# Optimization experiments

Measured on AMD Instinct MI355X. Metric: run time of the kernel, lower is better.

## Reference

```python
import jax, jax.numpy as jnp
import numpy as np

T, B, E, H = 1024, 64, 512, 512


def setup_inputs() -> dict:
    key = jax.random.key(0)
    ks = jax.random.split(key, 13)
    a = 1.0 / np.sqrt(H)
    u = lambda k, shape, lo=-a, hi=a: jax.random.uniform(k, shape, jnp.float32, lo, hi)
    return {
        "embeds": jax.random.normal(ks[0], (T, B, E), jnp.float32),
        "w_gx": u(ks[1], (E, H)), "w_gh": u(ks[2], (H, H)), "bias_g": u(ks[3], (H,)),
        "w_ix": u(ks[4], (E, H)), "w_ih": u(ks[5], (H, H)), "bias_i": u(ks[6], (H,)),
        "w_fx": u(ks[7], (E, H)), "w_fh": u(ks[8], (H, H)), "bias_f": u(ks[9], (H,), 1.0 - a, 1.0 + a),
        "w_ox": u(ks[10], (E, H)), "w_oh": u(ks[11], (H, H)), "bias_o": u(ks[12], (H,)),
    }


def reference(embeds, w_gx, w_gh, bias_g, w_ix, w_ih, bias_i,
              w_fx, w_fh, bias_f, w_ox, w_oh, bias_o):
    # Precompute all input projections in one big batched matmul: [T,B,4H]
    Wx = jnp.concatenate([w_gx, w_ix, w_fx, w_ox], axis=1)            # [E,4H]
    Wh = jnp.concatenate([w_gh, w_ih, w_fh, w_oh], axis=1)            # [H,4H]
    b = jnp.concatenate([bias_g, bias_i, bias_f, bias_o], axis=0)     # [4H]
    x_proj = jnp.einsum("tbe,ef->tbf", embeds, Wx) + b                # [T,B,4H]

    Bsz = embeds.shape[1]
    h0 = jnp.zeros((Bsz, H), embeds.dtype)
    c0 = jnp.zeros((Bsz, H), embeds.dtype)

    def step(carry, xp):
        h, c = carry
        z = xp + h @ Wh                                               # [B,4H]
        g = jnp.tanh(z[:, :H])
        i = jax.nn.sigmoid(z[:, H:2 * H])
        f = jax.nn.sigmoid(z[:, 2 * H:3 * H])
        o = jax.nn.sigmoid(z[:, 3 * H:])
        c_new = g * i + c * f
        h_new = jnp.tanh(c_new) * o
        return (h_new, c_new), h_new

    _, hs = jax.lax.scan(step, (h0, c0), x_proj)
    return hs  # [T,B,H]
```

## Files before the change

### kernel.cpp

```cpp
#include <hip/hip_runtime.h>
#include <stdint.h>
#include <stddef.h>


#define Tn 1024
#define Bn 64
#define Hn 512
#define En 512
#define NGROUP 4
#define NJBLK 32
#define NBLOCK (NGROUP * NJBLK)
#define POISON8 0x7F807F807F807F80ull
#define INIT8   0xAAAAAAAAAAAAAAAAull

using bf16x8 = __attribute__((ext_vector_type(8))) __bf16;
using f32x4  = __attribute__((ext_vector_type(4))) float;
using u16x8  = __attribute__((ext_vector_type(8))) unsigned short;
using u16x4  = __attribute__((ext_vector_type(4))) unsigned short;

__device__ __forceinline__ unsigned short f2bf(float f) {
    unsigned u = __builtin_bit_cast(unsigned, f);
    unsigned r = (u + 0x7FFFu + ((u >> 16) & 1u)) >> 16;
    return (unsigned short)r;
}
__device__ __forceinline__ float bf2f(unsigned short b) {
    unsigned u = ((unsigned)b) << 16;
    return __builtin_bit_cast(float, u);
}

__global__ __launch_bounds__(256, 1) void lstm_persistent(
    const float* __restrict__ embeds,
    const float* __restrict__ wx0, const float* __restrict__ wh0, const float* __restrict__ bs0,
    const float* __restrict__ wx1, const float* __restrict__ wh1, const float* __restrict__ bs1,
    const float* __restrict__ wx2, const float* __restrict__ wh2, const float* __restrict__ bs2,
    const float* __restrict__ wx3, const float* __restrict__ wh3, const float* __restrict__ bs3,
    float* __restrict__ out, void* __restrict__ ws)
{
    __shared__ unsigned short Xhi[16][520];
    __shared__ unsigned short Xlo[16][520];
    __shared__ unsigned short Hl[16][520];
    __shared__ float exch[4][16][17];

    const int tid  = threadIdx.x;
    const int wav  = tid >> 6;
    const int lane = tid & 63;
    const int q    = lane >> 4;
    const int n    = lane & 15;

    const int bidx = blockIdx.x;
    const int gid  = (bidx >> 1) & 3;
    const int kid  = ((bidx >> 3) << 1) | (bidx & 1);
    const int b0   = gid * 16;
    const int j0   = kid * 16;

    unsigned long long* gbase = (unsigned long long*)ws + (size_t)gid * 3 * 2048;

    const float* wxp = (wav == 0) ? wx0 : (wav == 1) ? wx1 : (wav == 2) ? wx2 : wx3;
    const float* whp = (wav == 0) ? wh0 : (wav == 1) ? wh1 : (wav == 2) ? wh2 : wh3;
    const float* bsp = (wav == 0) ? bs0 : (wav == 1) ? bs1 : (wav == 2) ? bs2 : bs3;

    bf16x8 WXhi[16], WXlo[16], WHhi[16], WHlo[16];
    const int col = j0 + n;
    #pragma unroll
    for (int kk = 0; kk < 16; ++kk) {
        u16x8 xh, xl, hh, hl;
        #pragma unroll
        for (int i = 0; i < 8; ++i) {
            int k = kk * 32 + q * 8 + i;
            float w  = wxp[(size_t)k * Hn + col];
            unsigned short hi = f2bf(w);
            xh[i] = hi;
            xl[i] = f2bf(w - bf2f(hi));
            w  = whp[(size_t)k * Hn + col];
            hi = f2bf(w);
            hh[i] = hi;
            hl[i] = f2bf(w - bf2f(hi));
        }
        WXhi[kk] = __builtin_bit_cast(bf16x8, xh);
        WXlo[kk] = __builtin_bit_cast(bf16x8, xl);
        WHhi[kk] = __builtin_bit_cast(bf16x8, hh);
        WHlo[kk] = __builtin_bit_cast(bf16x8, hl);
    }
    const float bias_l = bsp[col];
    float c_state = 0.f;
    const int b = tid >> 4, j = tid & 15;

    float4 xpre[8];
    #pragma unroll
    for (int it = 0; it < 8; ++it) {
        int idx = tid + it * 256;
        int r = idx >> 7, cc = idx & 127;
        xpre[it] = ((const float4*)(embeds + ((size_t)(b0 + r)) * En))[cc];
    }

    for (int t = 1; t <= Tn; ++t) {
        const int tau = t - 1;

        #pragma unroll
        for (int it = 0; it < 8; ++it) {
            int idx = tid + it * 256;
            int r = idx >> 7, cc = idx & 127;
            float4 v = xpre[it];
            float fs[4] = {v.x, v.y, v.z, v.w};
            u16x4 vh, vl;
            #pragma unroll
            for (int e = 0; e < 4; ++e) {
                unsigned short hb = f2bf(fs[e]);
                vh[e] = hb;
                vl[e] = f2bf(fs[e] - bf2f(hb));
            }
            *(u16x4*)&Xhi[r][cc * 4] = vh;
            *(u16x4*)&Xlo[r][cc * 4] = vl;
        }
        __syncthreads();

        unsigned long long hv8[8];
        unsigned long long* src = gbase + (size_t)((t - 1) % 3) * 2048;
        if (t > 1) {
            #pragma unroll
            for (int i = 0; i < 8; ++i)
                hv8[i] = __hip_atomic_load(src + tid + i * 256,
                                           __ATOMIC_RELAXED, __HIP_MEMORY_SCOPE_AGENT);
        }

        if (t < Tn) {
            #pragma unroll
            for (int it = 0; it < 8; ++it) {
                int idx = tid + it * 256;
                int r = idx >> 7, cc = idx & 127;
                xpre[it] = ((const float4*)(embeds + ((size_t)t * Bn + b0 + r) * En))[cc];
            }
        }

        f32x4 acc, acc2, acc3;
        acc[0] = bias_l; acc[1] = bias_l; acc[2] = bias_l; acc[3] = bias_l;
        acc2[0] = 0.f; acc2[1] = 0.f; acc2[2] = 0.f; acc2[3] = 0.f;
        acc3[0] = 0.f; acc3[1] = 0.f; acc3[2] = 0.f; acc3[3] = 0.f;

        #pragma unroll
        for (int kk = 0; kk < 16; ++kk) {
            bf16x8 ah = __builtin_bit_cast(bf16x8, *(const u16x8*)&Xhi[n][kk * 32 + q * 8]);
            bf16x8 al = __builtin_bit_cast(bf16x8, *(const u16x8*)&Xlo[n][kk * 32 + q * 8]);
            acc  = __builtin_amdgcn_mfma_f32_16x16x32_bf16(ah, WXhi[kk], acc, 0, 0, 0);
            acc2 = __builtin_amdgcn_mfma_f32_16x16x32_bf16(ah, WXlo[kk], acc2, 0, 0, 0);
            acc3 = __builtin_amdgcn_mfma_f32_16x16x32_bf16(al, WXhi[kk], acc3, 0, 0, 0);
        }

        if (t > 1) {
            int bad = 0;
            #pragma unroll
            for (int i = 0; i < 8; ++i)
                bad |= (hv8[i] == POISON8 || hv8[i] == INIT8) ? (1 << i) : 0;
            while (bad) {
                #pragma unroll
                for (int i = 0; i < 8; ++i)
                    if (bad & (1 << i))
                        hv8[i] = __hip_atomic_load(src + tid + i * 256,
                                                   __ATOMIC_RELAXED, __HIP_MEMORY_SCOPE_AGENT);
                int nb = 0;
                #pragma unroll
                for (int i = 0; i < 8; ++i)
                    nb |= (hv8[i] == POISON8 || hv8[i] == INIT8) ? (1 << i) : 0;
                bad = nb;
            }
            #pragma unroll
            for (int i = 0; i < 8; ++i) {
                int idx = tid + i * 256, r = idx >> 7, c8 = idx & 127;
                *(u16x4*)&Hl[r][c8 * 4] = __builtin_bit_cast(u16x4, hv8[i]);
            }
        }

        if (tid < 64) {
            int pr = tid >> 2, pq = tid & 3;
            __hip_atomic_store(gbase + (size_t)((t + 1) % 3) * 2048
                                   + pr * 128 + (j0 >> 2) + pq,
                               (unsigned long long)POISON8,
                               __ATOMIC_RELAXED, __HIP_MEMORY_SCOPE_AGENT);
        }

        if (t > 1) {
            __syncthreads();
            #pragma unroll
            for (int kk = 0; kk < 16; ++kk) {
                bf16x8 a = __builtin_bit_cast(bf16x8, *(const u16x8*)&Hl[n][kk * 32 + q * 8]);
                acc  = __builtin_amdgcn_mfma_f32_16x16x32_bf16(a, WHhi[kk], acc, 0, 0, 0);
                acc2 = __builtin_amdgcn_mfma_f32_16x16x32_bf16(a, WHlo[kk], acc2, 0, 0, 0);
            }
        }

        #pragma unroll
        for (int r = 0; r < 4; ++r) {
            float zv  = acc[r] + acc2[r] + acc3[r];
            float arg = (wav == 0) ? -2.f * zv : -zv;
            float s   = __builtin_amdgcn_rcpf(1.f + __expf(arg));
            float act = (wav == 0) ? (2.f * s - 1.f) : s;
            exch[wav][q * 4 + r][n] = act;
        }
        __syncthreads();

        float hv;
        {
            float g  = exch[0][b][j];
            float ig = exch[1][b][j];
            float fg = exch[2][b][j];
            float og = exch[3][b][j];
            c_state = g * ig + c_state * fg;
            float e2 = __expf(-2.f * c_state);
            float th = 2.f * __builtin_amdgcn_rcpf(1.f + e2) - 1.f;
            hv = th * og;
        }

        {
            unsigned pk = (unsigned)f2bf(hv);
            unsigned v1 = __shfl_down((int)pk, 1);
            unsigned v2 = __shfl_down((int)pk, 2);
            unsigned v3 = __shfl_down((int)pk, 3);
            if ((lane & 3) == 0 && t < Tn) {
                unsigned long long qv =
                    (unsigned long long)(pk | (v1 << 16))
                    | ((unsigned long long)(v2 | (v3 << 16)) << 32);
                __hip_atomic_store(gbase + (size_t)(t % 3) * 2048
                                       + b * 128 + (j0 >> 2) + (j >> 2),
                                   qv, __ATOMIC_RELAXED, __HIP_MEMORY_SCOPE_AGENT);
            }
        }

        out[((size_t)tau * Bn + b0 + b) * Hn + j0 + j] = hv;
    }
}

extern "C" void kernel_launch(void* const* d_in, const int* in_sizes, int n_in,
                              void* d_out, int out_size, void* d_ws, size_t ws_size,
                              hipStream_t stream) {
    lstm_persistent<<<dim3(NBLOCK), dim3(256), 0, stream>>>(
        (const float*)d_in[0],
        (const float*)d_in[1], (const float*)d_in[2], (const float*)d_in[3],
        (const float*)d_in[4], (const float*)d_in[5], (const float*)d_in[6],
        (const float*)d_in[7], (const float*)d_in[8], (const float*)d_in[9],
        (const float*)d_in[10], (const float*)d_in[11], (const float*)d_in[12],
        (float*)d_out, d_ws);
}
```

Baseline: 3.230 ms.

## Load hidden state straight into MFMA fragments and double-buffer the input tile

The global hidden-state exchange buffer is re-laid out in MFMA fragment order, so each lane atomically loads its own A-operand chunks into registers instead of staging them through shared memory. This drops the LDS write, a __syncthreads and the LDS reads from the recurrent path. The input embedding conversion is double-buffered one step ahead, which removes the per-step barrier before the X matmul. The hidden matmul also uses separate accumulators to shorten the dependency chain. In exchange, per-lane register pressure rises (32 u64 values) and the poll loop covers more loads.

```diff
diff --git a/kernel.cpp b/kernel.cpp
--- a/kernel.cpp
+++ b/kernel.cpp
@@ -17,6 +17,7 @@
 using f32x4  = __attribute__((ext_vector_type(4))) float;
 using u16x8  = __attribute__((ext_vector_type(8))) unsigned short;
 using u16x4  = __attribute__((ext_vector_type(4))) unsigned short;
+using u64x2  = __attribute__((ext_vector_type(2))) unsigned long long;
 
 __device__ __forceinline__ unsigned short f2bf(float f) {
     unsigned u = __builtin_bit_cast(unsigned, f);
@@ -26,6 +27,9 @@
 __device__ __forceinline__ float bf2f(unsigned short b) {
     unsigned u = ((unsigned)b) << 16;
     return __builtin_bit_cast(float, u);
+}
+__device__ __forceinline__ int chunk_idx(int c, int b) {
+    return ((c >> 5) << 7) + (((c >> 3) & 3) << 5) + (b << 1) + ((c >> 2) & 1);
 }
 
 __global__ __launch_bounds__(256, 1) void lstm_persistent(
@@ -36,9 +40,8 @@
     const float* __restrict__ wx3, const float* __restrict__ wh3, const float* __restrict__ bs3,
     float* __restrict__ out, void* __restrict__ ws)
 {
-    __shared__ unsigned short Xhi[16][520];
-    __shared__ unsigned short Xlo[16][520];
-    __shared__ unsigned short Hl[16][520];
+    __shared__ unsigned short Xhi[2][16][520];
+    __shared__ unsigned short Xlo[2][16][520];
     __shared__ float exch[4][16][17];
 
     const int tid  = threadIdx.x;
@@ -90,112 +93,135 @@
     for (int it = 0; it < 8; ++it) {
         int idx = tid + it * 256;
         int r = idx >> 7, cc = idx & 127;
-        xpre[it] = ((const float4*)(embeds + ((size_t)(b0 + r)) * En))[cc];
-    }
+        float4 v = ((const float4*)(embeds + ((size_t)(b0 + r)) * En))[cc];
+        float fs[4] = {v.x, v.y, v.z, v.w};
+        u16x4 vh, vl;
+        #pragma unroll
+        for (int e = 0; e < 4; ++e) {
+            unsigned short hb = f2bf(fs[e]);
+            vh[e] = hb;
+            vl[e] = f2bf(fs[e] - bf2f(hb));
+        }
+        *(u16x4*)&Xhi[1][r][cc * 4] = vh;
+        *(u16x4*)&Xlo[1][r][cc * 4] = vl;
+    }
+    #pragma unroll
+    for (int it = 0; it < 8; ++it) {
+        int idx = tid + it * 256;
+        int r = idx >> 7, cc = idx & 127;
+        xpre[it] = ((const float4*)(embeds + ((size_t)1 * Bn + b0 + r) * En))[cc];
+    }
+    __syncthreads();
 
     for (int t = 1; t <= Tn; ++t) {
         const int tau = t - 1;
-
-        #pragma unroll
-        for (int it = 0; it < 8; ++it) {
-            int idx = tid + it * 256;
-            int r = idx >> 7, cc = idx & 127;
-            float4 v = xpre[it];
-            float fs[4] = {v.x, v.y, v.z, v.w};
-            u16x4 vh, vl;
-            #pragma unroll
-            for (int e = 0; e < 4; ++e) {
-                unsigned short hb = f2bf(fs[e]);
-                vh[e] = hb;
-                vl[e] = f2bf(fs[e] - bf2f(hb));
-            }
-            *(u16x4*)&Xhi[r][cc * 4] = vh;
-            *(u16x4*)&Xlo[r][cc * 4] = vl;
-        }
-        __syncthreads();
-
-        unsigned long long hv8[8];
-        unsigned long long* src = gbase + (size_t)((t - 1) % 3) * 2048;
-        if (t > 1) {
-            #pragma unroll
-            for (int i = 0; i < 8; ++i)
-                hv8[i] = __hip_atomic_load(src + tid + i * 256,
-                                           __ATOMIC_RELAXED, __HIP_MEMORY_SCOPE_AGENT);
-        }
+        const int rbuf = t & 1;
+        const int wbuf = rbuf ^ 1;
 
         if (t < Tn) {
             #pragma unroll
             for (int it = 0; it < 8; ++it) {
                 int idx = tid + it * 256;
                 int r = idx >> 7, cc = idx & 127;
-                xpre[it] = ((const float4*)(embeds + ((size_t)t * Bn + b0 + r) * En))[cc];
-            }
-        }
-
-        f32x4 acc, acc2, acc3;
+                float4 v = xpre[it];
+                float fs[4] = {v.x, v.y, v.z, v.w};
+                u16x4 vh, vl;
+                #pragma unroll
+                for (int e = 0; e < 4; ++e) {
+                    unsigned short hb = f2bf(fs[e]);
+                    vh[e] = hb;
+                    vl[e] = f2bf(fs[e] - bf2f(hb));
+                }
+                *(u16x4*)&Xhi[wbuf][r][cc * 4] = vh;
+                *(u16x4*)&Xlo[wbuf][r][cc * 4] = vl;
+            }
+        }
+
+        unsigned long long hreg[32];
+        unsigned long long* src = gbase + (size_t)((t - 1) % 3) * 2048;
+        const int fbase = q * 32 + n * 2;
+        if (t > 1) {
+            #pragma unroll
+            for (int kk = 0; kk < 16; ++kk) {
+                hreg[2 * kk]     = __hip_atomic_load(src + kk * 128 + fbase,
+                                       __ATOMIC_RELAXED, __HIP_MEMORY_SCOPE_AGENT);
+                hreg[2 * kk + 1] = __hip_atomic_load(src + kk * 128 + fbase + 1,
+                                       __ATOMIC_RELAXED, __HIP_MEMORY_SCOPE_AGENT);
+            }
+        }
+
+        if (t + 1 < Tn) {
+            #pragma unroll
+            for (int it = 0; it < 8; ++it) {
+                int idx = tid + it * 256;
+                int r = idx >> 7, cc = idx & 127;
+                xpre[it] = ((const float4*)(embeds + ((size_t)(t + 1) * Bn + b0 + r) * En))[cc];
+            }
+        }
+
+        f32x4 acc, acc2, acc3, accH, accL;
         acc[0] = bias_l; acc[1] = bias_l; acc[2] = bias_l; acc[3] = bias_l;
         acc2[0] = 0.f; acc2[1] = 0.f; acc2[2] = 0.f; acc2[3] = 0.f;
         acc3[0] = 0.f; acc3[1] = 0.f; acc3[2] = 0.f; acc3[3] = 0.f;
+        accH = acc2; accL = acc2;
 
         #pragma unroll
         for (int kk = 0; kk < 16; ++kk) {
-            bf16x8 ah = __builtin_bit_cast(bf16x8, *(const u16x8*)&Xhi[n][kk * 32 + q * 8]);
-            bf16x8 al = __builtin_bit_cast(bf16x8, *(const u16x8*)&Xlo[n][kk * 32 + q * 8]);
+            bf16x8 ah = __builtin_bit_cast(bf16x8, *(const u16x8*)&Xhi[rbuf][n][kk * 32 + q * 8]);
+            bf16x8 al = __builtin_bit_cast(bf16x8, *(const u16x8*)&Xlo[rbuf][n][kk * 32 + q * 8]);
             acc  = __builtin_amdgcn_mfma_f32_16x16x32_bf16(ah, WXhi[kk], acc, 0, 0, 0);
             acc2 = __builtin_amdgcn_mfma_f32_16x16x32_bf16(ah, WXlo[kk], acc2, 0, 0, 0);
             acc3 = __builtin_amdgcn_mfma_f32_16x16x32_bf16(al, WXhi[kk], acc3, 0, 0, 0);
         }
 
         if (t > 1) {
-            int bad = 0;
-            #pragma unroll
-            for (int i = 0; i < 8; ++i)
-                bad |= (hv8[i] == POISON8 || hv8[i] == INIT8) ? (1 << i) : 0;
+            unsigned bad = 0;
+            #pragma unroll
+            for (int i = 0; i < 32; ++i)
+                bad |= (hreg[i] == POISON8 || hreg[i] == INIT8) ? (1u << i) : 0u;
             while (bad) {
                 #pragma unroll
-                for (int i = 0; i < 8; ++i)
-                    if (bad & (1 << i))
-                        hv8[i] = __hip_atomic_load(src + tid + i * 256,
-                                                   __ATOMIC_RELAXED, __HIP_MEMORY_SCOPE_AGENT);
-                int nb = 0;
+                for (int i = 0; i < 32; ++i)
+                    if (bad & (1u << i))
+                        hreg[i] = __hip_atomic_load(src + (i >> 1) * 128 + fbase + (i & 1),
+                                      __ATOMIC_RELAXED, __HIP_MEMORY_SCOPE_AGENT);
+                unsigned nb = 0;
                 #pragma unroll
-                for (int i = 0; i < 8; ++i)
-                    nb |= (hv8[i] == POISON8 || hv8[i] == INIT8) ? (1 << i) : 0;
+                for (int i = 0; i < 32; ++i)
+                    nb |= (hreg[i] == POISON8 || hreg[i] == INIT8) ? (1u << i) : 0u;
                 bad = nb;
             }
-            #pragma unroll
-            for (int i = 0; i < 8; ++i) {
-                int idx = tid + i * 256, r = idx >> 7, c8 = idx & 127;
-                *(u16x4*)&Hl[r][c8 * 4] = __builtin_bit_cast(u16x4, hv8[i]);
-            }
         }
 
         if (tid < 64) {
-            int pr = tid >> 2, pq = tid & 3;
+            int pb = tid >> 2, pq = tid & 3;
             __hip_atomic_store(gbase + (size_t)((t + 1) % 3) * 2048
-                                   + pr * 128 + (j0 >> 2) + pq,
+                                   + chunk_idx(j0 + pq * 4, pb),
                                (unsigned long long)POISON8,
                                __ATOMIC_RELAXED, __HIP_MEMORY_SCOPE_AGENT);
         }
 
         if (t > 1) {
-            __syncthreads();
             #pragma unroll
             for (int kk = 0; kk < 16; ++kk) {
-                bf16x8 a = __builtin_bit_cast(bf16x8, *(const u16x8*)&Hl[n][kk * 32 + q * 8]);
-                acc  = __builtin_amdgcn_mfma_f32_16x16x32_bf16(a, WHhi[kk], acc, 0, 0, 0);
-                acc2 = __builtin_amdgcn_mfma_f32_16x16x32_bf16(a, WHlo[kk], acc2, 0, 0, 0);
+                u64x2 p;
+                p[0] = hreg[2 * kk];
+                p[1] = hreg[2 * kk + 1];
+                bf16x8 a = __builtin_bit_cast(bf16x8, p);
+                accH = __builtin_amdgcn_mfma_f32_16x16x32_bf16(a, WHhi[kk], accH, 0, 0, 0);
+                accL = __builtin_amdgcn_mfma_f32_16x16x32_bf16(a, WHlo[kk], accL, 0, 0, 0);
             }
         }
 
         #pragma unroll
         for (int r = 0; r < 4; ++r) {
-            float zv  = acc[r] + acc2[r] + acc3[r];
+            float zv  = acc[r] + acc2[r] + acc3[r] + accH[r] + accL[r];
             float arg = (wav == 0) ? -2.f * zv : -zv;
             float s   = __builtin_amdgcn_rcpf(1.f + __expf(arg));
             float act = (wav == 0) ? (2.f * s - 1.f) : s;
             exch[wav][q * 4 + r][n] = act;
         }
+
         __syncthreads();
 
         float hv;
@@ -220,7 +246,7 @@
                     (unsigned long long)(pk | (v1 << 16))
                     | ((unsigned long long)(v2 | (v3 << 16)) << 32);
                 __hip_atomic_store(gbase + (size_t)(t % 3) * 2048
-                                       + b * 128 + (j0 >> 2) + (j >> 2),
+                                       + chunk_idx(j0 + (j & ~3), b),
                                    qv, __ATOMIC_RELAXED, __HIP_MEMORY_SCOPE_AGENT);
             }
         }
```

Result: slower. 5.438 ms (+68.4%).
